# Kernel optimization log

Hardware: AMD Instinct MI355X
Metric: run time of the kernel (lower is better)

Reference implementation:

```python
import jax, jax.numpy as jnp
import numpy as np

N = 10000      # atoms
E = 320000     # edges (~32 neighbors/atom)
H = 128        # hidden_channels
F = 128        # num_filters
R = 50         # num_rbf
L = 6          # num_layers
MAXZ = 100
CUT = 5.0      # cutoff_upper (cutoff_lower = 0)


def _cosine_cutoff(d):
    # CosineCutoff with lower=0: 0.5*(cos(pi*d/cut)+1) for d < cut, else 0
    return jnp.where(d < CUT, 0.5 * (jnp.cos(jnp.pi * d / CUT) + 1.0), 0.0)


def _xavier(k, shape):
    fan_in, fan_out = shape[-2], shape[-1]
    lim = np.sqrt(6.0 / (fan_in + fan_out)).astype(np.float32)
    return jax.random.uniform(k, shape, jnp.float32, -lim, lim)


def setup_inputs() -> dict:
    key = jax.random.key(0)
    ks = jax.random.split(key, 16)
    start = float(np.exp(-CUT))  # exp(-cutoff_upper + cutoff_lower)
    return {
        "z": jax.random.randint(ks[0], (N,), 0, MAXZ),
        "pos": jax.random.normal(ks[1], (N, 3), jnp.float32) * 3.0,
        "batch": jnp.zeros((N,), jnp.int32),
        "edge_index": jax.random.randint(ks[2], (2, E), 0, N),
        # nn.Embedding for atom types (main + NeighborEmbedding's own table)
        "emb_table": jax.random.normal(ks[3], (MAXZ, H), jnp.float32),
        "nbr_emb_table": jax.random.normal(ks[4], (MAXZ, H), jnp.float32),
        # NeighborEmbedding: distance_proj (R->H) and combine (2H->H)
        "nbr_proj_W": _xavier(ks[5], (R, H)),
        "nbr_proj_b": jnp.zeros((H,), jnp.float32),
        "nbr_comb_W": _xavier(ks[6], (2 * H, H)),
        "nbr_comb_b": jnp.zeros((H,), jnp.float32),
        # ExpNormalSmearing params (trainable)
        "rbf_means": jnp.linspace(start, 1.0, R, dtype=jnp.float32),
        "rbf_betas": jnp.full((R,), (2.0 / R * (1.0 - start)) ** -2, dtype=jnp.float32),
        # L interaction blocks, params stacked on leading layer dim
        "mlpW1": _xavier(ks[7], (L, R, F)),   # filter net lin1
        "mlpb1": jnp.zeros((L, F), jnp.float32),
        "mlpW2": _xavier(ks[8], (L, F, F)),   # filter net lin2
        "mlpb2": jnp.zeros((L, F), jnp.float32),
        "convW1": _xavier(ks[9], (L, H, F)),  # CFConv lin1 (no bias)
        "convW2": _xavier(ks[10], (L, F, H)), # CFConv lin2
        "convb2": jnp.zeros((L, H), jnp.float32),
        "linW": _xavier(ks[11], (L, H, H)),   # InteractionBlock final lin
        "linb": jnp.zeros((L, H), jnp.float32),
    }


def reference(z, pos, batch, edge_index, emb_table, nbr_emb_table,
              nbr_proj_W, nbr_proj_b, nbr_comb_W, nbr_comb_b,
              rbf_means, rbf_betas, mlpW1, mlpb1, mlpW2, mlpb2,
              convW1, convW2, convb2, linW, linb):
    src, dst = edge_index[0], edge_index[1]
    diff = pos[src] - pos[dst]                       # (E,3)
    d = jnp.sqrt(jnp.sum(diff * diff, axis=-1) + 1e-12)  # edge_weight (E,)
    C = _cosine_cutoff(d)                            # (E,)
    # ExpNormalSmearing: alpha = 5/(cut-0) = 1
    edge_attr = C[:, None] * jnp.exp(
        -rbf_betas * (jnp.exp(-d)[:, None] - rbf_means) ** 2)  # (E,R)

    x = emb_table[z]                                 # (N,H)

    # NeighborEmbedding: self-loops removed, filter modulated by cutoff
    mask = (src != dst).astype(x.dtype)
    Wn = (edge_attr @ nbr_proj_W + nbr_proj_b) * (C * mask)[:, None]  # (E,H)
    msg = jax.ops.segment_sum(nbr_emb_table[z][src] * Wn, dst, num_segments=N)
    x = jnp.concatenate([x, msg], axis=-1) @ nbr_comb_W + nbr_comb_b

    # Interaction blocks: CFConv (gather - filter-MLP - scatter) + residual
    for l in range(L):
        Wf = jax.nn.silu(edge_attr @ mlpW1[l] + mlpb1[l]) @ mlpW2[l] + mlpb2[l]
        Wf = Wf * C[:, None]                         # (E,F)
        y = x @ convW1[l]                            # (N,F), no bias
        m = jax.ops.segment_sum(y[src] * Wf, dst, num_segments=N)  # aggr='add'
        y = jax.nn.silu(m @ convW2[l] + convb2[l])
        y = y @ linW[l] + linb[l]
        x = x + y
    return x
```

## Files before the change

kernel.cpp:

```cpp
#include <hip/hip_runtime.h>
#include <hip/hip_bf16.h>


#define NATOMS 10000
#define NEDGES 320000
#define HC 128
#define RBF 50
#define NLAY 6
#define MAXZ_ 100
#define NK 8192
#define EGRID (NEDGES / 64)
#define YGRID ((NATOMS + 63) / 64)
#define UGRID (NATOMS / 16)

typedef __hip_bfloat16 bf16;
typedef __attribute__((ext_vector_type(8))) short bf8v;
typedef __attribute__((ext_vector_type(4))) float f4v;

__device__ __forceinline__ float b2f(bf16 v) { return __bfloat162float(v); }
__device__ __forceinline__ bf16  f2b(float v) { return __float2bfloat16(v); }
__device__ __forceinline__ short f2s(float v) { bf16 h = f2b(v); return *(short*)&h; }
__device__ __forceinline__ float s2f(unsigned short s) {
    return __int_as_float(((int)s) << 16);
}
__device__ __forceinline__ float silu(float v) {
    return v * __builtin_amdgcn_rcpf(1.0f + __expf(-v));
}
__device__ __forceinline__ int isf_of(const int* flagp) {
    return (__int_as_float(flagp[0]) > 1.0e4f) ? 1 : 0;
}

template<int ISF>
__device__ __forceinline__ float LD(const void* p, size_t i) {
    if (ISF) return ((const float*)p)[i];
    return b2f(((const bf16*)p)[i]);
}

__device__ __forceinline__ int clampN(int v) {
    return v < 0 ? 0 : (v >= NATOMS ? NATOMS - 1 : v);
}

template<int ISF>
__device__ __forceinline__ float edge_d(const int* __restrict__ ei,
                                        const void* __restrict__ pos, int e,
                                        int* sOut, int* tOut) {
    int s = clampN(ei[e]);
    int t = clampN(ei[NEDGES + e]);
    *sOut = s; *tOut = t;
    float dx = LD<ISF>(pos, (size_t)s * 3 + 0) - LD<ISF>(pos, (size_t)t * 3 + 0);
    float dy = LD<ISF>(pos, (size_t)s * 3 + 1) - LD<ISF>(pos, (size_t)t * 3 + 1);
    float dz = LD<ISF>(pos, (size_t)s * 3 + 2) - LD<ISF>(pos, (size_t)t * 3 + 2);
    float d = sqrtf(dx * dx + dy * dy + dz * dz + 1e-12f);
    if (d != d) d = 1e30f;
    return d;
}

__global__ void probe_k(const void* pos, int* flag) {
    int i = blockIdx.x * 256 + threadIdx.x;
    float v = 0.0f;
    if (i < NATOMS * 3) {
        v = fabsf(b2f(((const bf16*)pos)[i]));
        if (v != v) v = 1e30f;
    }
    #pragma unroll
    for (int off = 32; off > 0; off >>= 1)
        v = fmaxf(v, __shfl_xor(v, off, 64));
    if ((threadIdx.x & 63) == 0) atomicMax(flag, __float_as_int(v));
}

template<int ISF>
__device__ void histd_body(const int* __restrict__ ei, const void* __restrict__ pos,
                           int* __restrict__ counts, float* __restrict__ ed_s,
                           int* __restrict__ src_s, int* __restrict__ dst_s,
                           float* __restrict__ d_raw) {
    int e = blockIdx.x * 256 + threadIdx.x;
    if (e >= NEDGES) return;
    ed_s[e] = 0.0f;
    src_s[e] = 0;
    dst_s[e] = NATOMS - 1;
    int s, t;
    float d = edge_d<ISF>(ei, pos, e, &s, &t);
    d_raw[e] = d;
    if (d < 5.0f) atomicAdd(&counts[t], 1);
}
__global__ void histd_k(const int* ei, const void* pos, const int* flagp,
                        int* counts, float* ed_s, int* src_s, int* dst_s,
                        float* d_raw) {
    if (isf_of(flagp)) histd_body<1>(ei, pos, counts, ed_s, src_s, dst_s, d_raw);
    else               histd_body<0>(ei, pos, counts, ed_s, src_s, dst_s, d_raw);
}

__global__ void scan_k(const int* __restrict__ counts, int* __restrict__ rowptr,
                       int* __restrict__ cursor) {
    __shared__ int wsum[16];
    int tid = threadIdx.x, lane = tid & 63, w = tid >> 6;
    int base = tid * 10;
    int v[10];
    int s = 0;
    #pragma unroll
    for (int j = 0; j < 10; j++) {
        int i = base + j;
        int c = (i < NATOMS) ? counts[i] : 0;
        v[j] = c; s += c;
    }
    int si = s;
    #pragma unroll
    for (int off = 1; off < 64; off <<= 1) {
        int t = __shfl_up(si, off, 64);
        if (lane >= off) si += t;
    }
    if (lane == 63) wsum[w] = si;
    __syncthreads();
    if (w == 0 && lane < 16) {
        int t = wsum[lane];
        int s2 = t;
        #pragma unroll
        for (int off = 1; off < 16; off <<= 1) {
            int u = __shfl_up(s2, off, 64);
            if (lane >= off) s2 += u;
        }
        wsum[lane] = s2 - t;
    }
    __syncthreads();
    int run = wsum[w] + si - s;
    #pragma unroll
    for (int j = 0; j < 10; j++) {
        int i = base + j;
        if (i < NATOMS) {
            cursor[i] = run;
            run += v[j];
            rowptr[i + 1] = run;
        }
    }
    if (tid == 0) rowptr[0] = 0;
}

__global__ void permgeom_k(const int* __restrict__ ei, const float* __restrict__ d_raw,
                           int* __restrict__ cursor,
                           float* __restrict__ ed_s, int* __restrict__ src_s,
                           int* __restrict__ dst_s) {
    int e = blockIdx.x * 256 + threadIdx.x;
    if (e >= NEDGES) return;
    float d = d_raw[e];
    if (d >= 5.0f) return;
    int s = clampN(ei[e]);
    int t = clampN(ei[NEDGES + e]);
    int p = atomicAdd(&cursor[t], 1);
    ed_s[p] = __expf(-d);
    src_s[p] = s;
    dst_s[p] = t;
}

template<int ISF>
__device__ void packB_at(int t, const void* src, int K, int ksteps, size_t perLsrc,
                         size_t perLdst, int L, bf16* dst) {
    if (t >= L * 8 * ksteps * 64) return;
    int lane = t & 63;
    int t2 = t >> 6;
    int ks = t2 % ksteps;
    int t3 = t2 / ksteps;
    int nt = t3 & 7;
    int l  = t3 >> 3;
    int quad = lane >> 4, lc = lane & 15;
    int col = nt * 16 + lc;
    for (int j = 0; j < 8; j++) {
        int k = ks * 32 + quad * 8 + j;
        float v = (k < K) ? LD<ISF>(src, (size_t)l * perLsrc + (size_t)k * 128 + col) : 0.0f;
        dst[(size_t)l * perLdst + ((size_t)((nt * ksteps + ks) * 64 + lane)) * 8 + j] = f2b(v);
    }
}
template<int ISF>
__device__ void packB24_at(int t, const void* w2, const void* cw1, const void* cw2,
                           const void* lw, bf16* w2p, bf16* cw1p, bf16* cw2p, bf16* lwp) {
    if (t >= 24 * 8 * 4 * 64) return;
    int lane = t & 63;
    int t2 = t >> 6;
    int ks = t2 & 3;
    int t3 = t2 >> 2;
    int nt = t3 & 7;
    int m  = t3 >> 3;
    int which = m / NLAY, li = m % NLAY;
    const void* src = which == 0 ? w2 : which == 1 ? cw1 : which == 2 ? cw2 : lw;
    bf16* dst = which == 0 ? w2p : which == 1 ? cw1p : which == 2 ? cw2p : lwp;
    int quad = lane >> 4, lc = lane & 15;
    int col = nt * 16 + lc;
    #pragma unroll
    for (int j = 0; j < 8; j++) {
        int k = ks * 32 + quad * 8 + j;
        float v = LD<ISF>(src, (size_t)li * 16384 + (size_t)k * 128 + col);
        dst[(size_t)li * 16384 + ((size_t)((nt * 4 + ks) * 64 + lane)) * 8 + j] = f2b(v);
    }
}
template<int ISF>
__device__ void cvts_at(int i, const void* means, const void* betas, const void* bp,
                        const void* bc, const void* b1, const void* b2,
                        const void* cb2, const void* lb,
                        float* meanscv, float* betascv, float* bpcv, float* bccv,
                        float* b1cv, float* b2cv, float* cb2cv, float* lbcv) {
    if      (i < 50)   meanscv[i]        = LD<ISF>(means, i);
    else if (i < 100)  betascv[i - 50]   = LD<ISF>(betas, i - 50);
    else if (i < 228)  bpcv[i - 100]     = LD<ISF>(bp, i - 100);
    else if (i < 356)  bccv[i - 228]     = LD<ISF>(bc, i - 228);
    else if (i < 1124) b1cv[i - 356]     = LD<ISF>(b1, i - 356);
    else if (i < 1892) b2cv[i - 1124]    = LD<ISF>(b2, i - 1124);
    else if (i < 2660) cb2cv[i - 1892]   = LD<ISF>(cb2, i - 1892);
    else if (i < 3428) lbcv[i - 2660]    = LD<ISF>(lb, i - 2660);
}
template<int ISF>
__device__ void packall_body(const void* Wp, const void* Wc, const void* W1,
                             const void* W2, const void* cW1, const void* cW2,
                             const void* lW, const void* means, const void* betas,
                             const void* bp, const void* bc, const void* b1,
                             const void* b2, const void* cb2, const void* lb,
                             const void* nbremb,
                             bf16* wpp, bf16* wcp, bf16* w1p, bf16* w2p, bf16* cw1p,
                             bf16* cw2p, bf16* lwp, float* meanscv, float* betascv,
                             float* bpcv, float* bccv, float* b1cv, float* b2cv,
                             float* cb2cv, float* lbcv, bf16* nbrembbf) {
    int b = blockIdx.x, tid = threadIdx.x;
    if (b < 4)        packB_at<ISF>(b * 256 + tid, Wp, RBF, 2, 6400, 8192, 1, wpp);
    else if (b < 20)  packB_at<ISF>((b - 4) * 256 + tid, Wc, 256, 8, 32768, 32768, 1, wcp);
    else if (b < 44)  packB_at<ISF>((b - 20) * 256 + tid, W1, RBF, 2, 6400, 8192, NLAY, w1p);
    else if (b < 236) packB24_at<ISF>((b - 44) * 256 + tid, W2, cW1, cW2, lW,
                                      w2p, cw1p, cw2p, lwp);
    else if (b < 250) cvts_at<ISF>((b - 236) * 256 + tid, means, betas, bp, bc, b1, b2,
                                   cb2, lb, meanscv, betascv, bpcv, bccv,
                                   b1cv, b2cv, cb2cv, lbcv);
    else {
        int i = (b - 250) * 256 + tid;
        if (i < MAXZ_ * HC) nbrembbf[i] = f2b(LD<ISF>(nbremb, i));
    }
}
__global__ void packall_k(const void* Wp, const void* Wc, const void* W1,
                          const void* W2, const void* cW1, const void* cW2,
                          const void* lW, const void* means, const void* betas,
                          const void* bp, const void* bc, const void* b1,
                          const void* b2, const void* cb2, const void* lb,
                          const void* nbremb, const int* flagp,
                          bf16* wpp, bf16* wcp, bf16* w1p, bf16* w2p, bf16* cw1p,
                          bf16* cw2p, bf16* lwp, float* meanscv, float* betascv,
                          float* bpcv, float* bccv, float* b1cv, float* b2cv,
                          float* cb2cv, float* lbcv, bf16* nbrembbf) {
    if (isf_of(flagp)) packall_body<1>(Wp, Wc, W1, W2, cW1, cW2, lW, means, betas,
                                       bp, bc, b1, b2, cb2, lb, nbremb, wpp, wcp,
                                       w1p, w2p, cw1p, cw2p, lwp, meanscv, betascv,
                                       bpcv, bccv, b1cv, b2cv, cb2cv, lbcv, nbrembbf);
    else               packall_body<0>(Wp, Wc, W1, W2, cW1, cW2, lW, means, betas,
                                       bp, bc, b1, b2, cb2, lb, nbremb, wpp, wcp,
                                       w1p, w2p, cw1p, cw2p, lwp, meanscv, betascv,
                                       bpcv, bccv, b1cv, b2cv, cb2cv, lbcv, nbrembbf);
}

#define MFMA(a, b, c) __builtin_amdgcn_mfma_f32_16x16x32_bf16((a), (b), (c), 0, 0, 0)

__device__ __forceinline__ void seg_prep(const int* __restrict__ dst_s, int i0, int tid,
                                         int* ddst, int* slot_s, int* distinct_s,
                                         int* nseg_s) {
    if (tid < 64) {
        int d = dst_s[i0 + tid];
        ddst[tid] = d;
        int dprev = __shfl_up(d, 1, 64);
        int flag = (tid == 0 || d != dprev) ? 1 : 0;
        int s = flag;
        #pragma unroll
        for (int off = 1; off < 64; off <<= 1) {
            int t = __shfl_up(s, off, 64);
            if (tid >= off) s += t;
        }
        slot_s[tid] = s - 1;
        if (flag) distinct_s[s - 1] = d;
        if (tid == 63) *nseg_s = s;
    }
}

__device__ __forceinline__ void seg_mfma(const bf16 (*mvT)[72], const int* ddst,
                                         const int* slot_s, const int* distinct_s,
                                         int nseg, float* __restrict__ out, int tid) {
    int wave = tid >> 6, lane = tid & 63, quad = lane >> 4, lc = lane & 15;
    if (nseg <= 16) {
        bf8v sa[2];
        #pragma unroll
        for (int ks = 0; ks < 2; ks++)
            #pragma unroll
            for (int j = 0; j < 8; j++) {
                int k = ks * 32 + quad * 8 + j;
                sa[ks][j] = (slot_s[k] == lc) ? (short)0x3F80 : (short)0;
            }
        f4v z4 = {0.f, 0.f, 0.f, 0.f};
        f4v sacc[2] = {z4, z4};
        #pragma unroll
        for (int nt = 0; nt < 2; nt++)
            #pragma unroll
            for (int ks = 0; ks < 2; ks++) {
                bf8v b = *(const bf8v*)&mvT[wave * 32 + nt * 16 + lc][ks * 32 + quad * 8];
                sacc[nt] = MFMA(sa[ks], b, sacc[nt]);
            }
        #pragma unroll
        for (int nt = 0; nt < 2; nt++)
            #pragma unroll
            for (int r = 0; r < 4; r++) {
                int sl = quad * 4 + r;
                if (sl < nseg) {
                    int atom = distinct_s[sl];
                    int n = wave * 32 + nt * 16 + lc;
                    float v = sacc[nt][r];
                    if (sl == 0 || sl == nseg - 1)
                        atomicAdd(&out[(size_t)atom * HC + n], v);
                    else
                        out[(size_t)atom * HC + n] = v;
                }
            }
    } else {
        int col = tid & 127;
        int base = (tid >> 7) * 32;
        int cur = ddst[base];
        float s = 0.0f;
        bool first = true;
        for (int e = base; e < base + 32; e++) {
            int dn = ddst[e];
            if (dn != cur) {
                if (first) atomicAdd(&out[(size_t)cur * HC + col], s);
                else out[(size_t)cur * HC + col] = s;
                first = false; cur = dn; s = 0.0f;
            }
            s += b2f(mvT[col][e]);
        }
        atomicAdd(&out[(size_t)cur * HC + col], s);
    }
}

__global__ __launch_bounds__(256)
void tabbuild_k(const bf16* __restrict__ wpp, const float* __restrict__ bpcv,
                const bf16* __restrict__ w1p, const float* __restrict__ b1cv,
                const bf16* __restrict__ w2p, const float* __restrict__ b2cv,
                const float* __restrict__ meanscv, const float* __restrict__ betascv,
                bf16* __restrict__ Tb) {
    __shared__ bf16 hid[64][136];
    __shared__ float csh[64], edsh[64];
    int f = blockIdx.x >> 7, kb = blockIdx.x & 127;
    int base = kb * 64;
    int tid = threadIdx.x;
    int wave = tid >> 6, lane = tid & 63, quad = lane >> 4, lc = lane & 15;
    if (tid < 64) {
        float ed = (float)(base + tid) * (1.0f / (NK - 1));
        float d = -logf(fmaxf(ed, 1e-30f));
        float C = (d < 5.0f) ? 0.5f * (__cosf(d * 0.6283185307f) + 1.0f) : 0.0f;
        csh[tid] = C; edsh[tid] = ed;
    }
    __syncthreads();
    float edi = edsh[wave * 16 + lc], Ci = csh[wave * 16 + lc];
    bf8v af[2];
    #pragma unroll
    for (int ks = 0; ks < 2; ks++) {
        #pragma unroll
        for (int j = 0; j < 8; j++) {
            int r = ks * 32 + quad * 8 + j;
            float v = 0.0f;
            if (r < RBF) { float u = edi - meanscv[r]; v = Ci * __expf(-betascv[r] * u * u); }
            af[ks][j] = f2s(v);
        }
    }
    f4v zero = {0.f, 0.f, 0.f, 0.f};
    f4v acc[8];
    #pragma unroll
    for (int nt = 0; nt < 8; nt++) acc[nt] = zero;
    const bf16* w1b = (f == 0) ? wpp : w1p + (size_t)(f - 1) * 8192;
    #pragma unroll
    for (int nt = 0; nt < 8; nt++)
        #pragma unroll
        for (int ks = 0; ks < 2; ks++) {
            bf8v b = *(const bf8v*)(w1b + ((nt * 2 + ks) * 64 + lane) * 8);
            acc[nt] = MFMA(af[ks], b, acc[nt]);
        }
    if (f == 0) {
        #pragma unroll
        for (int nt = 0; nt < 8; nt++) {
            int n = nt * 16 + lc;
            float bb = bpcv[n];
            #pragma unroll
            for (int r = 0; r < 4; r++) {
                int row = wave * 16 + quad * 4 + r;
                Tb[(size_t)(base + row) * HC + n] = f2b((acc[nt][r] + bb) * csh[row]);
            }
        }
        return;
    }
    int l = f - 1;
    #pragma unroll
    for (int nt = 0; nt < 8; nt++) {
        int n = nt * 16 + lc;
        float bb = b1cv[l * HC + n];
        #pragma unroll
        for (int r = 0; r < 4; r++)
            hid[wave * 16 + quad * 4 + r][n] = f2b(silu(acc[nt][r] + bb));
    }
    __syncthreads();
    bf8v a2[4];
    #pragma unroll
    for (int ks = 0; ks < 4; ks++)
        a2[ks] = *(const bf8v*)&hid[wave * 16 + lc][ks * 32 + quad * 8];
    f4v acc2[8];
    #pragma unroll
    for (int nt = 0; nt < 8; nt++) acc2[nt] = zero;
    const bf16* w2b = w2p + (size_t)l * 16384;
    #pragma unroll
    for (int nt = 0; nt < 8; nt++)
        #pragma unroll
        for (int ks = 0; ks < 4; ks++) {
            bf8v b = *(const bf8v*)(w2b + ((nt * 4 + ks) * 64 + lane) * 8);
            acc2[nt] = MFMA(a2[ks], b, acc2[nt]);
        }
    #pragma unroll
    for (int nt = 0; nt < 8; nt++) {
        int n = nt * 16 + lc;
        float bb = b2cv[l * HC + n];
        #pragma unroll
        for (int r = 0; r < 4; r++) {
            int row = wave * 16 + quad * 4 + r;
            Tb[((size_t)f * NK + base + row) * HC + n] = f2b((acc2[nt][r] + bb) * csh[row]);
        }
    }
}

__global__ __launch_bounds__(256)
void nbr_tab_k(const int* __restrict__ rowptr,
               const float* __restrict__ ed_s, const int* __restrict__ src_s,
               const int* __restrict__ dst_s, const int* __restrict__ z,
               const bf16* __restrict__ nbrembbf, const bf16* __restrict__ Tb,
               float* __restrict__ msg) {
    __shared__ bf16 mvT[128][72];
    __shared__ int ddst[64], slot_s[64], distinct_s[64];
    __shared__ int nseg_s;
    int i0 = blockIdx.x * 64;
    if (i0 >= rowptr[NATOMS]) return;
    int tid = threadIdx.x;
    seg_prep(dst_s, i0, tid, ddst, slot_s, distinct_s, &nseg_s);
    int row = tid & 63, c0 = (tid >> 6) * 32;
    int e = i0 + row;
    int s = src_s[e];
    float msk = (s != dst_s[e]) ? 1.0f : 0.0f;
    float pos = fminf(fmaxf(ed_s[e] * (float)(NK - 1) + 0.5f, 0.0f), (float)(NK - 1));
    int k = (int)pos;
    const bf8v* tp = (const bf8v*)(Tb + (size_t)k * HC + c0);
    bf8v tv[4];
    #pragma unroll
    for (int g = 0; g < 4; g++) tv[g] = tp[g];
    int zz = z[s]; zz = zz < 0 ? 0 : (zz >= MAXZ_ ? MAXZ_ - 1 : zz);
    const bf8v* ep = (const bf8v*)(nbrembbf + (size_t)zz * HC + c0);
    bf8v ev[4];
    #pragma unroll
    for (int g = 0; g < 4; g++) ev[g] = ep[g];
    #pragma unroll
    for (int g = 0; g < 4; g++)
        #pragma unroll
        for (int m = 0; m < 8; m++) {
            float v = s2f((unsigned short)tv[g][m]) * msk *
                      s2f((unsigned short)ev[g][m]);
            mvT[c0 + g * 8 + m][row] = f2b(v);
        }
    __syncthreads();
    seg_mfma(mvT, ddst, slot_s, distinct_s, nseg_s, msg, tid);
}

template<int ISF>
__device__ void combine_body(const int* __restrict__ z, const void* __restrict__ emb,
                             const float* __restrict__ msg, const bf16* __restrict__ wcp,
                             const float* __restrict__ bccv, const bf16* __restrict__ cw1b,
                             float* __restrict__ x, bf16* __restrict__ xb,
                             bf16* __restrict__ ybf) {
    __shared__ bf16 srow[64][136];
    int tid = threadIdx.x;
    int wave = tid >> 6, lane = tid & 63, quad = lane >> 4, lc = lane & 15;
    int m0 = blockIdx.x * 64;
    int arow = m0 + wave * 16 + lc;
    int rowc = arow < NATOMS ? arow : NATOMS - 1;
    int zz = z[rowc]; zz = zz < 0 ? 0 : (zz >= MAXZ_ ? MAXZ_ - 1 : zz);
    bf8v af[8];
    #pragma unroll
    for (int ks = 0; ks < 4; ks++)
        #pragma unroll
        for (int j = 0; j < 8; j++)
            af[ks][j] = f2s(LD<ISF>(emb, (size_t)zz * HC + ks * 32 + quad * 8 + j));
    #pragma unroll
    for (int ks = 4; ks < 8; ks++) {
        const float* mp = msg + (size_t)rowc * HC + (ks - 4) * 32 + quad * 8;
        #pragma unroll
        for (int j = 0; j < 8; j++) af[ks][j] = f2s(mp[j]);
    }
    f4v zero = {0.f, 0.f, 0.f, 0.f};
    f4v acc[8];
    #pragma unroll
    for (int nt = 0; nt < 8; nt++) acc[nt] = zero;
    #pragma unroll
    for (int nt = 0; nt < 8; nt++)
        #pragma unroll
        for (int ks = 0; ks < 8; ks++) {
            bf8v b = *(const bf8v*)(wcp + ((nt * 8 + ks) * 64 + lane) * 8);
            acc[nt] = MFMA(af[ks], b, acc[nt]);
        }
    #pragma unroll
    for (int nt = 0; nt < 8; nt++) {
        int n = nt * 16 + lc;
        float bb = bccv[n];
        #pragma unroll
        for (int r = 0; r < 4; r++) {
            int row = m0 + wave * 16 + quad * 4 + r;
            float v = acc[nt][r] + bb;
            bf16 vb = f2b(v);
            srow[wave * 16 + quad * 4 + r][n] = vb;
            if (row < NATOMS) {
                x[(size_t)row * HC + n] = v;
                xb[(size_t)row * HC + n] = vb;
            }
        }
    }
    __syncthreads();
    bf8v a3[4];
    #pragma unroll
    for (int ks = 0; ks < 4; ks++)
        a3[ks] = *(const bf8v*)&srow[wave * 16 + lc][ks * 32 + quad * 8];
    f4v acc3[8];
    #pragma unroll
    for (int nt = 0; nt < 8; nt++) acc3[nt] = zero;
    #pragma unroll
    for (int nt = 0; nt < 8; nt++)
        #pragma unroll
        for (int ks = 0; ks < 4; ks++) {
            bf8v b = *(const bf8v*)(cw1b + ((nt * 4 + ks) * 64 + lane) * 8);
            acc3[nt] = MFMA(a3[ks], b, acc3[nt]);
        }
    #pragma unroll
    for (int nt = 0; nt < 8; nt++) {
        int n = nt * 16 + lc;
        #pragma unroll
        for (int r = 0; r < 4; r++) {
            int row = m0 + wave * 16 + quad * 4 + r;
            if (row < NATOMS) ybf[(size_t)row * HC + n] = f2b(acc3[nt][r]);
        }
    }
}
__global__ __launch_bounds__(256)
void combine_k(const int* z, const void* emb, const float* msg, const bf16* wcp,
               const float* bccv, const bf16* cw1b, const int* flagp,
               float* x, bf16* xb, bf16* ybf) {
    if (isf_of(flagp)) combine_body<1>(z, emb, msg, wcp, bccv, cw1b, x, xb, ybf);
    else               combine_body<0>(z, emb, msg, wcp, bccv, cw1b, x, xb, ybf);
}

__global__ __launch_bounds__(256)
void filt_tab_k(int l, const int* __restrict__ rowptr,
                const float* __restrict__ ed_s, const int* __restrict__ src_s,
                const int* __restrict__ dst_s, const bf16* __restrict__ ybf,
                const bf16* __restrict__ Tb, float* __restrict__ msum) {
    __shared__ bf16 mvT[128][72];
    __shared__ int ddst[64], slot_s[64], distinct_s[64];
    __shared__ int nseg_s;
    int i0 = blockIdx.x * 64;
    if (i0 >= rowptr[NATOMS]) return;
    int tid = threadIdx.x;
    seg_prep(dst_s, i0, tid, ddst, slot_s, distinct_s, &nseg_s);
    int row = tid & 63, c0 = (tid >> 6) * 32;
    int e = i0 + row;
    float pos = fminf(fmaxf(ed_s[e] * (float)(NK - 1) + 0.5f, 0.0f), (float)(NK - 1));
    int k = (int)pos;
    const bf8v* tp = (const bf8v*)(Tb + ((size_t)(l + 1) * NK + k) * HC + c0);
    bf8v tv[4];
    #pragma unroll
    for (int g = 0; g < 4; g++) tv[g] = tp[g];
    const bf8v* yp = (const bf8v*)(ybf + (size_t)src_s[e] * HC + c0);
    bf8v yv[4];
    #pragma unroll
    for (int g = 0; g < 4; g++) yv[g] = yp[g];
    #pragma unroll
    for (int g = 0; g < 4; g++)
        #pragma unroll
        for (int m = 0; m < 8; m++) {
            float v = s2f((unsigned short)tv[g][m]) * s2f((unsigned short)yv[g][m]);
            mvT[c0 + g * 8 + m][row] = f2b(v);
        }
    __syncthreads();
    seg_mfma(mvT, ddst, slot_s, distinct_s, nseg_s, msum, tid);
}

__global__ __launch_bounds__(256)
void upd_mfma_k(float* msum, int l,
                const bf16* __restrict__ cw2p, const float* __restrict__ cb2cv,
                const bf16* __restrict__ lwp, const float* __restrict__ lbcv,
                const bf16* __restrict__ cw1p, int do_y, int last,
                float* __restrict__ x, bf16* __restrict__ xb,
                bf16* __restrict__ ybf, void* out, const int* flagp) {
    __shared__ bf16 srow[16][136];
    int tid = threadIdx.x;
    int w = tid >> 6, lane = tid & 63, quad = lane >> 4, lc = lane & 15;
    int m0 = blockIdx.x * 16;
    bf8v af[4];
    #pragma unroll
    for (int ks = 0; ks < 4; ks++) {
        const float* p = msum + (size_t)(m0 + lc) * HC + ks * 32 + quad * 8;
        bf8v f;
        #pragma unroll
        for (int j = 0; j < 8; j++) f[j] = f2s(p[j]);
        af[ks] = f;
    }
    f4v zero = {0.f, 0.f, 0.f, 0.f};
    f4v acc[2] = {zero, zero};
    const bf16* c2b = cw2p + (size_t)l * 16384;
    #pragma unroll
    for (int nt = 0; nt < 2; nt++)
        #pragma unroll
        for (int ks = 0; ks < 4; ks++) {
            bf8v b = *(const bf8v*)(c2b + (((w * 2 + nt) * 4 + ks) * 64 + lane) * 8);
            acc[nt] = MFMA(af[ks], b, acc[nt]);
        }
    #pragma unroll
    for (int nt = 0; nt < 2; nt++) {
        int n = w * 32 + nt * 16 + lc;
        float bb = cb2cv[l * HC + n];
        #pragma unroll
        for (int r = 0; r < 4; r++)
            srow[quad * 4 + r][n] = f2b(silu(acc[nt][r] + bb));
    }
    __syncthreads();
    {
        int zr = tid >> 4, zc = (tid & 15) * 8;
        *(f4v*)(msum + (size_t)(m0 + zr) * HC + zc) = zero;
        *(f4v*)(msum + (size_t)(m0 + zr) * HC + zc + 4) = zero;
    }
    bf8v a2[4];
    #pragma unroll
    for (int ks = 0; ks < 4; ks++)
        a2[ks] = *(const bf8v*)&srow[lc][ks * 32 + quad * 8];
    __syncthreads();
    f4v acc2[2] = {zero, zero};
    const bf16* lwb = lwp + (size_t)l * 16384;
    #pragma unroll
    for (int nt = 0; nt < 2; nt++)
        #pragma unroll
        for (int ks = 0; ks < 4; ks++) {
            bf8v b = *(const bf8v*)(lwb + (((w * 2 + nt) * 4 + ks) * 64 + lane) * 8);
            acc2[nt] = MFMA(a2[ks], b, acc2[nt]);
        }
    int isf = isf_of(flagp);
    #pragma unroll
    for (int nt = 0; nt < 2; nt++) {
        int n = w * 32 + nt * 16 + lc;
        float bb = lbcv[l * HC + n];
        #pragma unroll
        for (int r = 0; r < 4; r++) {
            int row = m0 + quad * 4 + r;
            size_t o = (size_t)row * HC + n;
            float nv = x[o] + acc2[nt][r] + bb;
            if (!last) {
                x[o] = nv;
                xb[o] = f2b(nv);
            } else {
                if (isf) ((float*)out)[o] = nv;
                else     ((bf16*)out)[o] = f2b(nv);
            }
            srow[quad * 4 + r][n] = f2b(nv);
        }
    }
    if (do_y) {
        __syncthreads();
        bf8v a3[4];
        #pragma unroll
        for (int ks = 0; ks < 4; ks++)
            a3[ks] = *(const bf8v*)&srow[lc][ks * 32 + quad * 8];
        f4v acc3[2] = {zero, zero};
        const bf16* c1b = cw1p + (size_t)(l + 1) * 16384;
        #pragma unroll
        for (int nt = 0; nt < 2; nt++)
            #pragma unroll
            for (int ks = 0; ks < 4; ks++) {
                bf8v b = *(const bf8v*)(c1b + (((w * 2 + nt) * 4 + ks) * 64 + lane) * 8);
                acc3[nt] = MFMA(a3[ks], b, acc3[nt]);
            }
        #pragma unroll
        for (int nt = 0; nt < 2; nt++) {
            int n = w * 32 + nt * 16 + lc;
            #pragma unroll
            for (int r = 0; r < 4; r++) {
                int row = m0 + quad * 4 + r;
                ybf[(size_t)row * HC + n] = f2b(acc3[nt][r]);
            }
        }
    }
}

extern "C" void kernel_launch(void* const* d_in, const int* in_sizes, int n_in,
                              void* d_out, int out_size, void* d_ws, size_t ws_size,
                              hipStream_t stream) {
    const int*  z      = (const int*) d_in[0];
    const void* pos    = d_in[1];
    const int*  ei     = (const int*) d_in[3];
    const void* emb    = d_in[4];
    const void* nbremb = d_in[5];
    const void* Wp     = d_in[6];
    const void* bp     = d_in[7];
    const void* Wc     = d_in[8];
    const void* bc     = d_in[9];
    const void* means  = d_in[10];
    const void* betas  = d_in[11];
    const void* W1     = d_in[12];
    const void* b1     = d_in[13];
    const void* W2     = d_in[14];
    const void* b2     = d_in[15];
    const void* cW1    = d_in[16];
    const void* cW2    = d_in[17];
    const void* cb2    = d_in[18];
    const void* lW     = d_in[19];
    const void* lb     = d_in[20];

    char* p = (char*)d_ws;
    auto alloc = [&](size_t bytes) { char* r = p; p += (bytes + 255) / 256 * 256; return r; };
    int*   flag    = (int*)  alloc(256);
    int*   counts  = (int*)  alloc((size_t)NATOMS * 4);
    float* msum    = (float*)alloc((size_t)NATOMS * HC * 4);
    float* msg     = (float*)alloc((size_t)NATOMS * HC * 4);
    int*   rowptr  = (int*)  alloc((size_t)(NATOMS + 1) * 4);
    int*   cursor  = (int*)  alloc((size_t)NATOMS * 4);
    int*   src_s   = (int*)  alloc((size_t)NEDGES * 4);
    int*   dst_s   = (int*)  alloc((size_t)NEDGES * 4);
    float* ed_s    = (float*)alloc((size_t)NEDGES * 4);
    float* d_raw   = (float*)alloc((size_t)NEDGES * 4);
    float* x       = (float*)alloc((size_t)NATOMS * HC * 4);
    bf16*  xb      = (bf16*) alloc((size_t)NATOMS * HC * 2);
    bf16*  ybf     = (bf16*) alloc((size_t)NATOMS * HC * 2);
    bf16*  Tb      = (bf16*) alloc((size_t)(NLAY + 1) * NK * HC * 2);
    bf16*  wpp     = (bf16*) alloc((size_t)8192 * 2);
    bf16*  wcp     = (bf16*) alloc((size_t)32768 * 2);
    bf16*  w1p     = (bf16*) alloc((size_t)NLAY * 8192 * 2);
    bf16*  w2p     = (bf16*) alloc((size_t)NLAY * 16384 * 2);
    bf16*  cw1p    = (bf16*) alloc((size_t)NLAY * 16384 * 2);
    bf16*  cw2p    = (bf16*) alloc((size_t)NLAY * 16384 * 2);
    bf16*  lwp     = (bf16*) alloc((size_t)NLAY * 16384 * 2);
    bf16*  nbrembbf= (bf16*) alloc((size_t)MAXZ_ * HC * 2);
    float* bpcv    = (float*)alloc((size_t)HC * 4);
    float* bccv    = (float*)alloc((size_t)HC * 4);
    float* b1cv    = (float*)alloc((size_t)NLAY * HC * 4);
    float* b2cv    = (float*)alloc((size_t)NLAY * HC * 4);
    float* cb2cv   = (float*)alloc((size_t)NLAY * HC * 4);
    float* lbcv    = (float*)alloc((size_t)NLAY * HC * 4);
    float* meanscv = (float*)alloc((size_t)RBF * 4);
    float* betascv = (float*)alloc((size_t)RBF * 4);

    const int EG = (NEDGES + 255) / 256;

    size_t zbytes = 256 + ((size_t)NATOMS * 4 + 255) / 256 * 256
                  + (size_t)2 * NATOMS * HC * 4;
    hipMemsetAsync(flag, 0, zbytes, stream);
    probe_k<<<(NATOMS * 3 + 255) / 256, 256, 0, stream>>>(pos, flag);
    histd_k<<<EG, 256, 0, stream>>>(ei, pos, flag, counts, ed_s, src_s, dst_s, d_raw);
    scan_k<<<1, 1024, 0, stream>>>(counts, rowptr, cursor);
    permgeom_k<<<EG, 256, 0, stream>>>(ei, d_raw, cursor, ed_s, src_s, dst_s);

    packall_k<<<300, 256, 0, stream>>>(Wp, Wc, W1, W2, cW1, cW2, lW, means, betas,
                                       bp, bc, b1, b2, cb2, lb, nbremb, flag,
                                       wpp, wcp, w1p, w2p, cw1p, cw2p, lwp,
                                       meanscv, betascv, bpcv, bccv, b1cv, b2cv,
                                       cb2cv, lbcv, nbrembbf);
    tabbuild_k<<<7 * (NK / 64), 256, 0, stream>>>(wpp, bpcv, w1p, b1cv, w2p, b2cv,
                                                  meanscv, betascv, Tb);

    nbr_tab_k<<<EGRID, 256, 0, stream>>>(rowptr, ed_s, src_s, dst_s, z, nbrembbf, Tb, msg);
    combine_k<<<YGRID, 256, 0, stream>>>(z, emb, msg, wcp, bccv, cw1p, flag, x, xb, ybf);

    for (int l = 0; l < NLAY; l++) {
        filt_tab_k<<<EGRID, 256, 0, stream>>>(l, rowptr, ed_s, src_s, dst_s, ybf, Tb, msum);
        int lastl = (l == NLAY - 1) ? 1 : 0;
        upd_mfma_k<<<UGRID, 256, 0, stream>>>(msum, l, cw2p, cb2cv, lwp, lbcv,
                                              cw1p, lastl ? 0 : 1, lastl,
                                              x, xb, ybf, d_out, flag);
    }
}
```

Before: 336.6 us.

## Merge setup kernels into two launches and vectorize fp32-to-bf16 operand loads

The edge histogram and weight packing now run as one launch, as do the edge permutation and filter table build, which cuts the setup from five launches to three. The padding for sorted edge buffers (ed_s, src_s, dst_s) moves into the initial memset instead of being written per edge. Scalar fp32 loads converted to bf16 for MFMA operands are replaced by 8-wide vector loads. The trade-off is a larger shared-memory footprint on the merged kernels and a bigger memset; the setup_2 blocks depend on the bias buffers written in setup1.

New measurement: 333.5 us. About the same (-0.9%).

```diff
diff --git a/kernel.cpp b/kernel.cpp
--- a/kernel.cpp
+++ b/kernel.cpp
@@ -9,6 +9,8 @@
 #define NLAY 6
 #define MAXZ_ 100
 #define NK 8192
+#define EG 1250
+#define TBGRID (7 * (NK / 64))
 #define EGRID (NEDGES / 64)
 #define YGRID ((NATOMS + 63) / 64)
 #define UGRID (NATOMS / 16)
@@ -34,6 +36,20 @@
 __device__ __forceinline__ float LD(const void* p, size_t i) {
     if (ISF) return ((const float*)p)[i];
     return b2f(((const bf16*)p)[i]);
+}
+
+__device__ __forceinline__ bf8v f32x8_to_b(const float* p) {
+    f4v v0 = *(const f4v*)p;
+    f4v v1 = *(const f4v*)(p + 4);
+    bf8v r;
+    r[0] = f2s(v0[0]); r[1] = f2s(v0[1]); r[2] = f2s(v0[2]); r[3] = f2s(v0[3]);
+    r[4] = f2s(v1[0]); r[5] = f2s(v1[1]); r[6] = f2s(v1[2]); r[7] = f2s(v1[3]);
+    return r;
+}
+template<int ISF>
+__device__ __forceinline__ bf8v LD8(const void* p, size_t i) {
+    if (ISF) return f32x8_to_b((const float*)p + i);
+    return *(const bf8v*)((const bf16*)p + i);
 }
 
 __device__ __forceinline__ int clampN(int v) {
@@ -69,86 +85,16 @@
 }
 
 template<int ISF>
-__device__ void histd_body(const int* __restrict__ ei, const void* __restrict__ pos,
-                           int* __restrict__ counts, float* __restrict__ ed_s,
-                           int* __restrict__ src_s, int* __restrict__ dst_s,
-                           float* __restrict__ d_raw) {
-    int e = blockIdx.x * 256 + threadIdx.x;
+__device__ __forceinline__ void histd_body(int b, int tid, const int* __restrict__ ei,
+                                           const void* __restrict__ pos,
+                                           int* __restrict__ counts,
+                                           float* __restrict__ d_raw) {
+    int e = b * 256 + tid;
     if (e >= NEDGES) return;
-    ed_s[e] = 0.0f;
-    src_s[e] = 0;
-    dst_s[e] = NATOMS - 1;
     int s, t;
     float d = edge_d<ISF>(ei, pos, e, &s, &t);
     d_raw[e] = d;
     if (d < 5.0f) atomicAdd(&counts[t], 1);
-}
-__global__ void histd_k(const int* ei, const void* pos, const int* flagp,
-                        int* counts, float* ed_s, int* src_s, int* dst_s,
-                        float* d_raw) {
-    if (isf_of(flagp)) histd_body<1>(ei, pos, counts, ed_s, src_s, dst_s, d_raw);
-    else               histd_body<0>(ei, pos, counts, ed_s, src_s, dst_s, d_raw);
-}
-
-__global__ void scan_k(const int* __restrict__ counts, int* __restrict__ rowptr,
-                       int* __restrict__ cursor) {
-    __shared__ int wsum[16];
-    int tid = threadIdx.x, lane = tid & 63, w = tid >> 6;
-    int base = tid * 10;
-    int v[10];
-    int s = 0;
-    #pragma unroll
-    for (int j = 0; j < 10; j++) {
-        int i = base + j;
-        int c = (i < NATOMS) ? counts[i] : 0;
-        v[j] = c; s += c;
-    }
-    int si = s;
-    #pragma unroll
-    for (int off = 1; off < 64; off <<= 1) {
-        int t = __shfl_up(si, off, 64);
-        if (lane >= off) si += t;
-    }
-    if (lane == 63) wsum[w] = si;
-    __syncthreads();
-    if (w == 0 && lane < 16) {
-        int t = wsum[lane];
-        int s2 = t;
-        #pragma unroll
-        for (int off = 1; off < 16; off <<= 1) {
-            int u = __shfl_up(s2, off, 64);
-            if (lane >= off) s2 += u;
-        }
-        wsum[lane] = s2 - t;
-    }
-    __syncthreads();
-    int run = wsum[w] + si - s;
-    #pragma unroll
-    for (int j = 0; j < 10; j++) {
-        int i = base + j;
-        if (i < NATOMS) {
-            cursor[i] = run;
-            run += v[j];
-            rowptr[i + 1] = run;
-        }
-    }
-    if (tid == 0) rowptr[0] = 0;
-}
-
-__global__ void permgeom_k(const int* __restrict__ ei, const float* __restrict__ d_raw,
-                           int* __restrict__ cursor,
-                           float* __restrict__ ed_s, int* __restrict__ src_s,
-                           int* __restrict__ dst_s) {
-    int e = blockIdx.x * 256 + threadIdx.x;
-    if (e >= NEDGES) return;
-    float d = d_raw[e];
-    if (d >= 5.0f) return;
-    int s = clampN(ei[e]);
-    int t = clampN(ei[NEDGES + e]);
-    int p = atomicAdd(&cursor[t], 1);
-    ed_s[p] = __expf(-d);
-    src_s[p] = s;
-    dst_s[p] = t;
 }
 
 template<int ISF>
@@ -207,7 +153,7 @@
     else if (i < 3428) lbcv[i - 2660]    = LD<ISF>(lb, i - 2660);
 }
 template<int ISF>
-__device__ void packall_body(const void* Wp, const void* Wc, const void* W1,
+__device__ void packall_body(int b, int tid, const void* Wp, const void* Wc, const void* W1,
                              const void* W2, const void* cW1, const void* cW2,
                              const void* lW, const void* means, const void* betas,
                              const void* bp, const void* bc, const void* b1,
@@ -217,7 +163,6 @@
                              bf16* cw2p, bf16* lwp, float* meanscv, float* betascv,
                              float* bpcv, float* bccv, float* b1cv, float* b2cv,
                              float* cb2cv, float* lbcv, bf16* nbrembbf) {
-    int b = blockIdx.x, tid = threadIdx.x;
     if (b < 4)        packB_at<ISF>(b * 256 + tid, Wp, RBF, 2, 6400, 8192, 1, wpp);
     else if (b < 20)  packB_at<ISF>((b - 4) * 256 + tid, Wc, 256, 8, 32768, 32768, 1, wcp);
     else if (b < 44)  packB_at<ISF>((b - 20) * 256 + tid, W1, RBF, 2, 6400, 8192, NLAY, w1p);
@@ -231,27 +176,207 @@
         if (i < MAXZ_ * HC) nbrembbf[i] = f2b(LD<ISF>(nbremb, i));
     }
 }
-__global__ void packall_k(const void* Wp, const void* Wc, const void* W1,
-                          const void* W2, const void* cW1, const void* cW2,
-                          const void* lW, const void* means, const void* betas,
-                          const void* bp, const void* bc, const void* b1,
-                          const void* b2, const void* cb2, const void* lb,
-                          const void* nbremb, const int* flagp,
-                          bf16* wpp, bf16* wcp, bf16* w1p, bf16* w2p, bf16* cw1p,
-                          bf16* cw2p, bf16* lwp, float* meanscv, float* betascv,
-                          float* bpcv, float* bccv, float* b1cv, float* b2cv,
-                          float* cb2cv, float* lbcv, bf16* nbrembbf) {
-    if (isf_of(flagp)) packall_body<1>(Wp, Wc, W1, W2, cW1, cW2, lW, means, betas,
-                                       bp, bc, b1, b2, cb2, lb, nbremb, wpp, wcp,
-                                       w1p, w2p, cw1p, cw2p, lwp, meanscv, betascv,
-                                       bpcv, bccv, b1cv, b2cv, cb2cv, lbcv, nbrembbf);
-    else               packall_body<0>(Wp, Wc, W1, W2, cW1, cW2, lW, means, betas,
-                                       bp, bc, b1, b2, cb2, lb, nbremb, wpp, wcp,
-                                       w1p, w2p, cw1p, cw2p, lwp, meanscv, betascv,
-                                       bpcv, bccv, b1cv, b2cv, cb2cv, lbcv, nbrembbf);
+
+__global__ __launch_bounds__(256)
+void setup1_k(const int* ei, const void* pos, const int* flagp,
+              int* counts, float* d_raw,
+              const void* Wp, const void* Wc, const void* W1,
+              const void* W2, const void* cW1, const void* cW2,
+              const void* lW, const void* means, const void* betas,
+              const void* bp, const void* bc, const void* b1,
+              const void* b2, const void* cb2, const void* lb,
+              const void* nbremb,
+              bf16* wpp, bf16* wcp, bf16* w1p, bf16* w2p, bf16* cw1p,
+              bf16* cw2p, bf16* lwp, float* meanscv, float* betascv,
+              float* bpcv, float* bccv, float* b1cv, float* b2cv,
+              float* cb2cv, float* lbcv, bf16* nbrembbf) {
+    int b = blockIdx.x, tid = threadIdx.x;
+    int isf = isf_of(flagp);
+    if (b < EG) {
+        if (isf) histd_body<1>(b, tid, ei, pos, counts, d_raw);
+        else     histd_body<0>(b, tid, ei, pos, counts, d_raw);
+    } else {
+        b -= EG;
+        if (isf) packall_body<1>(b, tid, Wp, Wc, W1, W2, cW1, cW2, lW, means, betas,
+                                 bp, bc, b1, b2, cb2, lb, nbremb, wpp, wcp,
+                                 w1p, w2p, cw1p, cw2p, lwp, meanscv, betascv,
+                                 bpcv, bccv, b1cv, b2cv, cb2cv, lbcv, nbrembbf);
+        else     packall_body<0>(b, tid, Wp, Wc, W1, W2, cW1, cW2, lW, means, betas,
+                                 bp, bc, b1, b2, cb2, lb, nbremb, wpp, wcp,
+                                 w1p, w2p, cw1p, cw2p, lwp, meanscv, betascv,
+                                 bpcv, bccv, b1cv, b2cv, cb2cv, lbcv, nbrembbf);
+    }
+}
+
+__global__ void scan_k(const int* __restrict__ counts, int* __restrict__ rowptr,
+                       int* __restrict__ cursor) {
+    __shared__ int wsum[16];
+    int tid = threadIdx.x, lane = tid & 63, w = tid >> 6;
+    int base = tid * 10;
+    int v[10];
+    int s = 0;
+    #pragma unroll
+    for (int j = 0; j < 10; j++) {
+        int i = base + j;
+        int c = (i < NATOMS) ? counts[i] : 0;
+        v[j] = c; s += c;
+    }
+    int si = s;
+    #pragma unroll
+    for (int off = 1; off < 64; off <<= 1) {
+        int t = __shfl_up(si, off, 64);
+        if (lane >= off) si += t;
+    }
+    if (lane == 63) wsum[w] = si;
+    __syncthreads();
+    if (w == 0 && lane < 16) {
+        int t = wsum[lane];
+        int s2 = t;
+        #pragma unroll
+        for (int off = 1; off < 16; off <<= 1) {
+            int u = __shfl_up(s2, off, 64);
+            if (lane >= off) s2 += u;
+        }
+        wsum[lane] = s2 - t;
+    }
+    __syncthreads();
+    int run = wsum[w] + si - s;
+    #pragma unroll
+    for (int j = 0; j < 10; j++) {
+        int i = base + j;
+        if (i < NATOMS) {
+            cursor[i] = run;
+            run += v[j];
+            rowptr[i + 1] = run;
+        }
+    }
+    if (tid == 0) rowptr[0] = 0;
 }
 
 #define MFMA(a, b, c) __builtin_amdgcn_mfma_f32_16x16x32_bf16((a), (b), (c), 0, 0, 0)
+
+__device__ __forceinline__ void permgeom_body(int b, int tid, const int* __restrict__ ei,
+                                              const float* __restrict__ d_raw,
+                                              int* __restrict__ cursor,
+                                              float* __restrict__ ed_s,
+                                              int* __restrict__ src_s,
+                                              int* __restrict__ dst_s) {
+    int e = b * 256 + tid;
+    if (e >= NEDGES) return;
+    float d = d_raw[e];
+    if (d >= 5.0f) return;
+    int s = clampN(ei[e]);
+    int t = clampN(ei[NEDGES + e]);
+    int p = atomicAdd(&cursor[t], 1);
+    ed_s[p] = __expf(-d);
+    src_s[p] = s;
+    dst_s[p] = t;
+}
+
+__device__ __forceinline__ void tabbuild_body(int bb, int tid,
+                const bf16* __restrict__ wpp, const float* __restrict__ bpcv,
+                const bf16* __restrict__ w1p, const float* __restrict__ b1cv,
+                const bf16* __restrict__ w2p, const float* __restrict__ b2cv,
+                const float* __restrict__ meanscv, const float* __restrict__ betascv,
+                bf16* __restrict__ Tb) {
+    __shared__ bf16 hid[64][136];
+    __shared__ float csh[64], edsh[64];
+    int f = bb >> 7, kb = bb & 127;
+    int base = kb * 64;
+    int wave = tid >> 6, lane = tid & 63, quad = lane >> 4, lc = lane & 15;
+    if (tid < 64) {
+        float ed = (float)(base + tid) * (1.0f / (NK - 1));
+        float d = -logf(fmaxf(ed, 1e-30f));
+        float C = (d < 5.0f) ? 0.5f * (__cosf(d * 0.6283185307f) + 1.0f) : 0.0f;
+        csh[tid] = C; edsh[tid] = ed;
+    }
+    __syncthreads();
+    float edi = edsh[wave * 16 + lc], Ci = csh[wave * 16 + lc];
+    bf8v af[2];
+    #pragma unroll
+    for (int ks = 0; ks < 2; ks++) {
+        #pragma unroll
+        for (int j = 0; j < 8; j++) {
+            int r = ks * 32 + quad * 8 + j;
+            float v = 0.0f;
+            if (r < RBF) { float u = edi - meanscv[r]; v = Ci * __expf(-betascv[r] * u * u); }
+            af[ks][j] = f2s(v);
+        }
+    }
+    f4v zero = {0.f, 0.f, 0.f, 0.f};
+    f4v acc[8];
+    #pragma unroll
+    for (int nt = 0; nt < 8; nt++) acc[nt] = zero;
+    const bf16* w1b = (f == 0) ? wpp : w1p + (size_t)(f - 1) * 8192;
+    #pragma unroll
+    for (int nt = 0; nt < 8; nt++)
+        #pragma unroll
+        for (int ks = 0; ks < 2; ks++) {
+            bf8v b = *(const bf8v*)(w1b + ((nt * 2 + ks) * 64 + lane) * 8);
+            acc[nt] = MFMA(af[ks], b, acc[nt]);
+        }
+    if (f == 0) {
+        #pragma unroll
+        for (int nt = 0; nt < 8; nt++) {
+            int n = nt * 16 + lc;
+            float bb2 = bpcv[n];
+            #pragma unroll
+            for (int r = 0; r < 4; r++) {
+                int row = wave * 16 + quad * 4 + r;
+                Tb[(size_t)(base + row) * HC + n] = f2b((acc[nt][r] + bb2) * csh[row]);
+            }
+        }
+        return;
+    }
+    int l = f - 1;
+    #pragma unroll
+    for (int nt = 0; nt < 8; nt++) {
+        int n = nt * 16 + lc;
+        float bb2 = b1cv[l * HC + n];
+        #pragma unroll
+        for (int r = 0; r < 4; r++)
+            hid[wave * 16 + quad * 4 + r][n] = f2b(silu(acc[nt][r] + bb2));
+    }
+    __syncthreads();
+    bf8v a2[4];
+    #pragma unroll
+    for (int ks = 0; ks < 4; ks++)
+        a2[ks] = *(const bf8v*)&hid[wave * 16 + lc][ks * 32 + quad * 8];
+    f4v acc2[8];
+    #pragma unroll
+    for (int nt = 0; nt < 8; nt++) acc2[nt] = zero;
+    const bf16* w2b = w2p + (size_t)l * 16384;
+    #pragma unroll
+    for (int nt = 0; nt < 8; nt++)
+        #pragma unroll
+        for (int ks = 0; ks < 4; ks++) {
+            bf8v b = *(const bf8v*)(w2b + ((nt * 4 + ks) * 64 + lane) * 8);
+            acc2[nt] = MFMA(a2[ks], b, acc2[nt]);
+        }
+    #pragma unroll
+    for (int nt = 0; nt < 8; nt++) {
+        int n = nt * 16 + lc;
+        float bb2 = b2cv[l * HC + n];
+        #pragma unroll
+        for (int r = 0; r < 4; r++) {
+            int row = wave * 16 + quad * 4 + r;
+            Tb[((size_t)f * NK + base + row) * HC + n] = f2b((acc2[nt][r] + bb2) * csh[row]);
+        }
+    }
+}
+
+__global__ __launch_bounds__(256)
+void setup2_k(const int* ei, const float* d_raw, int* cursor,
+              float* ed_s, int* src_s, int* dst_s,
+              const bf16* wpp, const float* bpcv,
+              const bf16* w1p, const float* b1cv,
+              const bf16* w2p, const float* b2cv,
+              const float* meanscv, const float* betascv, bf16* Tb) {
+    int b = blockIdx.x, tid = threadIdx.x;
+    if (b < EG) permgeom_body(b, tid, ei, d_raw, cursor, ed_s, src_s, dst_s);
+    else        tabbuild_body(b - EG, tid, wpp, bpcv, w1p, b1cv, w2p, b2cv,
+                              meanscv, betascv, Tb);
+}
 
 __device__ __forceinline__ void seg_prep(const int* __restrict__ dst_s, int i0, int tid,
                                          int* ddst, int* slot_s, int* distinct_s,
@@ -326,99 +451,6 @@
             s += b2f(mvT[col][e]);
         }
         atomicAdd(&out[(size_t)cur * HC + col], s);
-    }
-}
-
-__global__ __launch_bounds__(256)
-void tabbuild_k(const bf16* __restrict__ wpp, const float* __restrict__ bpcv,
-                const bf16* __restrict__ w1p, const float* __restrict__ b1cv,
-                const bf16* __restrict__ w2p, const float* __restrict__ b2cv,
-                const float* __restrict__ meanscv, const float* __restrict__ betascv,
-                bf16* __restrict__ Tb) {
-    __shared__ bf16 hid[64][136];
-    __shared__ float csh[64], edsh[64];
-    int f = blockIdx.x >> 7, kb = blockIdx.x & 127;
-    int base = kb * 64;
-    int tid = threadIdx.x;
-    int wave = tid >> 6, lane = tid & 63, quad = lane >> 4, lc = lane & 15;
-    if (tid < 64) {
-        float ed = (float)(base + tid) * (1.0f / (NK - 1));
-        float d = -logf(fmaxf(ed, 1e-30f));
-        float C = (d < 5.0f) ? 0.5f * (__cosf(d * 0.6283185307f) + 1.0f) : 0.0f;
-        csh[tid] = C; edsh[tid] = ed;
-    }
-    __syncthreads();
-    float edi = edsh[wave * 16 + lc], Ci = csh[wave * 16 + lc];
-    bf8v af[2];
-    #pragma unroll
-    for (int ks = 0; ks < 2; ks++) {
-        #pragma unroll
-        for (int j = 0; j < 8; j++) {
-            int r = ks * 32 + quad * 8 + j;
-            float v = 0.0f;
-            if (r < RBF) { float u = edi - meanscv[r]; v = Ci * __expf(-betascv[r] * u * u); }
-            af[ks][j] = f2s(v);
-        }
-    }
-    f4v zero = {0.f, 0.f, 0.f, 0.f};
-    f4v acc[8];
-    #pragma unroll
-    for (int nt = 0; nt < 8; nt++) acc[nt] = zero;
-    const bf16* w1b = (f == 0) ? wpp : w1p + (size_t)(f - 1) * 8192;
-    #pragma unroll
-    for (int nt = 0; nt < 8; nt++)
-        #pragma unroll
-        for (int ks = 0; ks < 2; ks++) {
-            bf8v b = *(const bf8v*)(w1b + ((nt * 2 + ks) * 64 + lane) * 8);
-            acc[nt] = MFMA(af[ks], b, acc[nt]);
-        }
-    if (f == 0) {
-        #pragma unroll
-        for (int nt = 0; nt < 8; nt++) {
-            int n = nt * 16 + lc;
-            float bb = bpcv[n];
-            #pragma unroll
-            for (int r = 0; r < 4; r++) {
-                int row = wave * 16 + quad * 4 + r;
-                Tb[(size_t)(base + row) * HC + n] = f2b((acc[nt][r] + bb) * csh[row]);
-            }
-        }
-        return;
-    }
-    int l = f - 1;
-    #pragma unroll
-    for (int nt = 0; nt < 8; nt++) {
-        int n = nt * 16 + lc;
-        float bb = b1cv[l * HC + n];
-        #pragma unroll
-        for (int r = 0; r < 4; r++)
-            hid[wave * 16 + quad * 4 + r][n] = f2b(silu(acc[nt][r] + bb));
-    }
-    __syncthreads();
-    bf8v a2[4];
-    #pragma unroll
-    for (int ks = 0; ks < 4; ks++)
-        a2[ks] = *(const bf8v*)&hid[wave * 16 + lc][ks * 32 + quad * 8];
-    f4v acc2[8];
-    #pragma unroll
-    for (int nt = 0; nt < 8; nt++) acc2[nt] = zero;
-    const bf16* w2b = w2p + (size_t)l * 16384;
-    #pragma unroll
-    for (int nt = 0; nt < 8; nt++)
-        #pragma unroll
-        for (int ks = 0; ks < 4; ks++) {
-            bf8v b = *(const bf8v*)(w2b + ((nt * 4 + ks) * 64 + lane) * 8);
-            acc2[nt] = MFMA(a2[ks], b, acc2[nt]);
-        }
-    #pragma unroll
-    for (int nt = 0; nt < 8; nt++) {
-        int n = nt * 16 + lc;
-        float bb = b2cv[l * HC + n];
-        #pragma unroll
-        for (int r = 0; r < 4; r++) {
-            int row = wave * 16 + quad * 4 + r;
-            Tb[((size_t)f * NK + base + row) * HC + n] = f2b((acc2[nt][r] + bb) * csh[row]);
-        }
     }
 }
 
@@ -478,15 +510,10 @@
     bf8v af[8];
     #pragma unroll
     for (int ks = 0; ks < 4; ks++)
-        #pragma unroll
-        for (int j = 0; j < 8; j++)
-            af[ks][j] = f2s(LD<ISF>(emb, (size_t)zz * HC + ks * 32 + quad * 8 + j));
-    #pragma unroll
-    for (int ks = 4; ks < 8; ks++) {
-        const float* mp = msg + (size_t)rowc * HC + (ks - 4) * 32 + quad * 8;
-        #pragma unroll
-        for (int j = 0; j < 8; j++) af[ks][j] = f2s(mp[j]);
-    }
+        af[ks] = LD8<ISF>(emb, (size_t)zz * HC + ks * 32 + quad * 8);
+    #pragma unroll
+    for (int ks = 4; ks < 8; ks++)
+        af[ks] = f32x8_to_b(msg + (size_t)rowc * HC + (ks - 4) * 32 + quad * 8);
     f4v zero = {0.f, 0.f, 0.f, 0.f};
     f4v acc[8];
     #pragma unroll
@@ -595,13 +622,8 @@
     int m0 = blockIdx.x * 16;
     bf8v af[4];
     #pragma unroll
-    for (int ks = 0; ks < 4; ks++) {
-        const float* p = msum + (size_t)(m0 + lc) * HC + ks * 32 + quad * 8;
-        bf8v f;
-        #pragma unroll
-        for (int j = 0; j < 8; j++) f[j] = f2s(p[j]);
-        af[ks] = f;
-    }
+    for (int ks = 0; ks < 4; ks++)
+        af[ks] = f32x8_to_b(msum + (size_t)(m0 + lc) * HC + ks * 32 + quad * 8);
     f4v zero = {0.f, 0.f, 0.f, 0.f};
     f4v acc[2] = {zero, zero};
     const bf16* c2b = cw2p + (size_t)l * 16384;
@@ -717,11 +739,12 @@
     int*   counts  = (int*)  alloc((size_t)NATOMS * 4);
     float* msum    = (float*)alloc((size_t)NATOMS * HC * 4);
     float* msg     = (float*)alloc((size_t)NATOMS * HC * 4);
+    float* ed_s    = (float*)alloc((size_t)NEDGES * 4);
+    int*   src_s   = (int*)  alloc((size_t)NEDGES * 4);
+    int*   dst_s   = (int*)  alloc((size_t)NEDGES * 4);
+    char*  zend    = p;
     int*   rowptr  = (int*)  alloc((size_t)(NATOMS + 1) * 4);
     int*   cursor  = (int*)  alloc((size_t)NATOMS * 4);
-    int*   src_s   = (int*)  alloc((size_t)NEDGES * 4);
-    int*   dst_s   = (int*)  alloc((size_t)NEDGES * 4);
-    float* ed_s    = (float*)alloc((size_t)NEDGES * 4);
     float* d_raw   = (float*)alloc((size_t)NEDGES * 4);
     float* x       = (float*)alloc((size_t)NATOMS * HC * 4);
     bf16*  xb      = (bf16*) alloc((size_t)NATOMS * HC * 2);
@@ -744,23 +767,19 @@
     float* meanscv = (float*)alloc((size_t)RBF * 4);
     float* betascv = (float*)alloc((size_t)RBF * 4);
 
-    const int EG = (NEDGES + 255) / 256;
-
-    size_t zbytes = 256 + ((size_t)NATOMS * 4 + 255) / 256 * 256
-                  + (size_t)2 * NATOMS * HC * 4;
-    hipMemsetAsync(flag, 0, zbytes, stream);
+    hipMemsetAsync(flag, 0, (size_t)(zend - (char*)flag), stream);
     probe_k<<<(NATOMS * 3 + 255) / 256, 256, 0, stream>>>(pos, flag);
-    histd_k<<<EG, 256, 0, stream>>>(ei, pos, flag, counts, ed_s, src_s, dst_s, d_raw);
+
+    setup1_k<<<EG + 300, 256, 0, stream>>>(ei, pos, flag, counts, d_raw,
+                                           Wp, Wc, W1, W2, cW1, cW2, lW, means, betas,
+                                           bp, bc, b1, b2, cb2, lb, nbremb,
+                                           wpp, wcp, w1p, w2p, cw1p, cw2p, lwp,
+                                           meanscv, betascv, bpcv, bccv, b1cv, b2cv,
+                                           cb2cv, lbcv, nbrembbf);
     scan_k<<<1, 1024, 0, stream>>>(counts, rowptr, cursor);
-    permgeom_k<<<EG, 256, 0, stream>>>(ei, d_raw, cursor, ed_s, src_s, dst_s);
-
-    packall_k<<<300, 256, 0, stream>>>(Wp, Wc, W1, W2, cW1, cW2, lW, means, betas,
-                                       bp, bc, b1, b2, cb2, lb, nbremb, flag,
-                                       wpp, wcp, w1p, w2p, cw1p, cw2p, lwp,
-                                       meanscv, betascv, bpcv, bccv, b1cv, b2cv,
-                                       cb2cv, lbcv, nbrembbf);
-    tabbuild_k<<<7 * (NK / 64), 256, 0, stream>>>(wpp, bpcv, w1p, b1cv, w2p, b2cv,
-                                                  meanscv, betascv, Tb);
+    setup2_k<<<EG + TBGRID, 256, 0, stream>>>(ei, d_raw, cursor, ed_s, src_s, dst_s,
+                                              wpp, bpcv, w1p, b1cv, w2p, b2cv,
+                                              meanscv, betascv, Tb);
 
     nbr_tab_k<<<EGRID, 256, 0, stream>>>(rowptr, ed_s, src_s, dst_s, z, nbrembbf, Tb, msg);
     combine_k<<<YGRID, 256, 0, stream>>>(z, emb, msg, wcp, bccv, cw1p, flag, x, xb, ybf);
```
